# Kernel tuning notes

Hardware: AMD Instinct MI355X
Metric: run time of the kernel (lower is better)

Reference implementation:

```python
import jax, jax.numpy as jnp
import numpy as np

N_SRC = 50000
N_DST = 50000
E = 500000
H = 128
ED = 32
EPS = 1e-5


def _linear_params(key, fan_in, fan_out):
    kw, kb = jax.random.split(key)
    bound = 1.0 / np.sqrt(fan_in)
    W = jax.random.uniform(kw, (fan_in, fan_out), jnp.float32, -bound, bound)
    b = jax.random.uniform(kb, (fan_out,), jnp.float32, -bound, bound)
    return W, b


def setup_inputs() -> dict:
    key = jax.random.key(0)
    ks = jax.random.split(key, 12)
    src_x = jax.random.normal(ks[0], (N_SRC, H), jnp.float32)
    dst_x = jax.random.normal(ks[1], (N_DST, H), jnp.float32)
    edge_index = jax.random.randint(ks[2], (2, E), 0, N_DST, jnp.int64)
    edge_attr = jax.random.normal(ks[3], (E, ED), jnp.float32)
    Wsrc, bsrc = _linear_params(ks[4], H, H)
    Wdst, bdst = _linear_params(ks[5], H, H)
    We, be = _linear_params(ks[6], ED, H)
    Wattn, battn = _linear_params(ks[7], 3 * H, 1)
    Wmsg, bmsg = _linear_params(ks[8], H, H)
    Wout, bout = _linear_params(ks[9], 2 * H, H)
    gamma = jnp.ones((H,), jnp.float32)
    beta = jnp.zeros((H,), jnp.float32)
    return dict(src_x=src_x, dst_x=dst_x, edge_index=edge_index, edge_attr=edge_attr,
                Wsrc=Wsrc, bsrc=bsrc, Wdst=Wdst, bdst=bdst, We=We, be=be,
                Wattn=Wattn, battn=battn, Wmsg=Wmsg, bmsg=bmsg,
                Wout=Wout, bout=bout, gamma=gamma, beta=beta)


def _segment_softmax(scores, idx, num_segments):
    # numerically stable softmax over variable-size segments of dst index
    m = jax.ops.segment_max(scores, idx, num_segments=num_segments)
    ex = jnp.exp(scores - m[idx])
    s = jax.ops.segment_sum(ex, idx, num_segments=num_segments)
    return ex / s[idx]


def reference(src_x, dst_x, edge_index, edge_attr,
              Wsrc, bsrc, Wdst, bdst, We, be,
              Wattn, battn, Wmsg, bmsg, Wout, bout, gamma, beta):
    src_idx = edge_index[0]
    dst_idx = edge_index[1]
    num_dst = dst_x.shape[0]

    src_feat = src_x[src_idx] @ Wsrc + bsrc          # [E, H]
    dst_feat = dst_x[dst_idx] @ Wdst + bdst          # [E, H]
    e_feat = edge_attr @ We + be                     # [E, H]

    attn_in = jnp.concatenate([src_feat, dst_feat, e_feat], axis=-1)  # [E, 3H]
    msg = (src_feat + e_feat) @ Wmsg + bmsg          # [E, H]

    scores = (jnp.tanh(attn_in) @ Wattn + battn)[:, 0]  # [E]
    alpha = _segment_softmax(scores, dst_idx, num_dst)   # [E]

    agg = jax.ops.segment_sum(msg * alpha[:, None], dst_idx, num_segments=num_dst)  # [num_dst, H]

    updated = jnp.concatenate([dst_x, agg], axis=-1) @ Wout + bout
    # dropout is identity in eval mode
    h = dst_x + updated
    mu = jnp.mean(h, axis=-1, keepdims=True)
    var = jnp.var(h, axis=-1, keepdims=True)
    return (h - mu) * jax.lax.rsqrt(var + EPS) * gamma + beta
```

## Files before the change

kernel.cpp:

```cpp
#include <hip/hip_runtime.h>
#include <math.h>

#define NSRC 50000
#define NDST 50000
#define NE   500000
#define HD   128
#define EDIM 32
#define LN_EPS 1e-5f

typedef __attribute__((ext_vector_type(8))) short short8;
typedef __attribute__((ext_vector_type(4))) float f32x4;
typedef unsigned short u16;

#define TL2E 2.8853900817779268f
#define L2E  1.4426950408889634f

__device__ __forceinline__ float EXP2(float x) {
#if __has_builtin(__builtin_amdgcn_exp2f)
    return __builtin_amdgcn_exp2f(x);
#else
    return exp2f(x);
#endif
}
__device__ __forceinline__ float RCP(float x) {
#if __has_builtin(__builtin_amdgcn_rcpf)
    return __builtin_amdgcn_rcpf(x);
#else
    return 1.f / x;
#endif
}
__device__ __forceinline__ u16 f2b(float x) {
    unsigned u = __float_as_uint(x);
    return (u16)((u + 0x7FFFu + ((u >> 16) & 1u)) >> 16);
}
__device__ __forceinline__ float b2f(u16 h) {
    return __uint_as_float(((unsigned)h) << 16);
}
__device__ __forceinline__ short8 ld8(const u16* p) { return *(const short8*)p; }

__global__ __launch_bounds__(128) void fold1_kernel(
    const float* __restrict__ Wsrc, const float* __restrict__ bsrc,
    const float* __restrict__ We,   const float* __restrict__ be,
    const float* __restrict__ Wmsg, const float* __restrict__ bmsg,
    float* __restrict__ Wsm, float* __restrict__ bsm,
    float* __restrict__ WeMsg, float* __restrict__ c2)
{
    const int j = threadIdx.x;
    const int r = blockIdx.x;
    float s = 0.f;
    if (r < 128) {
        for (int k = 0; k < 128; ++k) s += Wsrc[r*HD + k] * Wmsg[k*HD + j];
        Wsm[r*HD + j] = s;
    } else if (r < 160) {
        const int rr = r - 128;
        for (int k = 0; k < 128; ++k) s += We[rr*HD + k] * Wmsg[k*HD + j];
        WeMsg[rr*HD + j] = s;
    } else if (r == 160) {
        for (int k = 0; k < 128; ++k) s += bsrc[k] * Wmsg[k*HD + j];
        bsm[j] = s + bmsg[j];
    } else {
        for (int k = 0; k < 128; ++k) s += be[k] * Wmsg[k*HD + j];
        c2[j] = s;
    }
}

__global__ __launch_bounds__(128) void fold2_kernel(
    const float* __restrict__ WeMsg, const float* __restrict__ c2,
    const float* __restrict__ Wout, const float* __restrict__ bout,
    float* __restrict__ W3, float* __restrict__ bias2,
    float* __restrict__ Wout1p)
{
    const int j = threadIdx.x;
    const int r = blockIdx.x;
    const float* Wout2 = Wout + HD*HD;
    if (r < 32) {
        float s = 0.f;
        for (int k = 0; k < 128; ++k) s += WeMsg[r*HD + k] * Wout2[k*HD + j];
        W3[r*HD + j] = s;
    } else if (r == 32) {
        float s = 0.f;
        for (int k = 0; k < 128; ++k) s += c2[k] * Wout2[k*HD + j];
        bias2[j] = s + bout[j];
    } else {
        const int rr = r - 33;
        Wout1p[rr*HD + j] = Wout[rr*HD + j] + ((rr == j) ? 1.f : 0.f);
    }
}

__global__ __launch_bounds__(64) void pack_all_kernel(
    const float* __restrict__ Wsrc, const float* __restrict__ Wdst,
    const float* __restrict__ Wsm,  const float* __restrict__ Wout1p,
    const float* __restrict__ Wout2,const float* __restrict__ We,
    const float* __restrict__ W3,
    u16* __restrict__ Wsrc_pk, u16* __restrict__ Wdst_pk,
    u16* __restrict__ Wsm_pk,  u16* __restrict__ W1_pk,
    u16* __restrict__ W2_pk,   u16* __restrict__ We_pk,
    u16* __restrict__ W3_pk)
{
    const int b = blockIdx.x;
    const int lane = threadIdx.x;
    const float* src; u16* dst; int lb; float scl = 1.f;
    if      (b < 32)  { src = Wsrc;   dst = Wsrc_pk; lb = b;       scl = TL2E; }
    else if (b < 64)  { src = Wdst;   dst = Wdst_pk; lb = b - 32;  scl = TL2E; }
    else if (b < 96)  { src = Wsm;    dst = Wsm_pk;  lb = b - 64; }
    else if (b < 128) { src = Wout1p; dst = W1_pk;   lb = b - 96; }
    else if (b < 160) { src = Wout2;  dst = W2_pk;   lb = b - 128; }
    else if (b < 168) { src = We;     dst = We_pk;   lb = b - 160; scl = TL2E; }
    else              { src = W3;     dst = W3_pk;   lb = b - 168; }
    const int kc = lb >> 3, t = lb & 7;
    const int ln = lane & 15, quad = lane >> 4;
    u16 tmp[8];
#pragma unroll
    for (int j = 0; j < 8; ++j)
        tmp[j] = f2b(src[(kc*32 + quad*8 + j)*HD + t*16 + ln] * scl);
    *(short8*)(dst + (size_t)(lb*64 + lane)*8) = *(short8*)tmp;
}

__global__ __launch_bounds__(256) void node_gemm_kernel(
    const float* __restrict__ src_x, const u16* __restrict__ Wsrc_pk,
    const u16* __restrict__ Wsm_pk, const float* __restrict__ bsrc,
    const float* __restrict__ bsm, const float* __restrict__ wa1,
    float* __restrict__ s1, u16* __restrict__ srcmsgb)
{
    __shared__ u16 lds[4 * 16 * HD];
    const int t = threadIdx.x;
    const int w = t >> 6, lane = t & 63;
    const int ln = lane & 15, quad = lane >> 4;
    int row0 = (blockIdx.x * 4 + w) * 16;
    if (row0 > NSRC - 16) row0 = NSRC - 16;

    const float* rp = src_x + (size_t)(row0 + ln)*HD;
    short8 a[4];
#pragma unroll
    for (int kc = 0; kc < 4; ++kc) {
        float4 f0 = *(const float4*)(rp + kc*32 + quad*8);
        float4 f1 = *(const float4*)(rp + kc*32 + quad*8 + 4);
        u16 tb[8] = { f2b(f0.x), f2b(f0.y), f2b(f0.z), f2b(f0.w),
                      f2b(f1.x), f2b(f1.y), f2b(f1.z), f2b(f1.w) };
        a[kc] = *(short8*)tb;
    }

    float v[4] = {0.f, 0.f, 0.f, 0.f};
    float ws = 0.f;
#pragma unroll
    for (int tt = 0; tt < 8; ++tt) {
        const float bb = bsrc[tt*16 + ln] * TL2E;
        const float ww = wa1[tt*16 + ln];
        f32x4 acc = {bb, bb, bb, bb};
#pragma unroll
        for (int kc = 0; kc < 4; ++kc) {
            short8 b = ld8(Wsrc_pk + (size_t)((kc*8 + tt)*64 + lane)*8);
            acc = __builtin_amdgcn_mfma_f32_16x16x32_bf16(a[kc], b, acc, 0, 0, 0);
        }
        ws += ww;
#pragma unroll
        for (int r = 0; r < 4; ++r)
            v[r] = fmaf(ww, RCP(EXP2(acc[r]) + 1.f), v[r]);
    }
#pragma unroll
    for (int off = 8; off >= 1; off >>= 1) {
        ws += __shfl_xor(ws, off);
#pragma unroll
        for (int r = 0; r < 4; ++r) v[r] += __shfl_xor(v[r], off);
    }
    if (ln == 0) {
#pragma unroll
        for (int r = 0; r < 4; ++r)
            s1[row0 + quad*4 + r] = fmaf(-2.f, v[r], ws);
    }

#pragma unroll
    for (int tt = 0; tt < 8; ++tt) {
        const float bs = bsm[tt*16 + ln];
        f32x4 acc = {bs, bs, bs, bs};
#pragma unroll
        for (int kc = 0; kc < 4; ++kc) {
            short8 b = ld8(Wsm_pk + (size_t)((kc*8 + tt)*64 + lane)*8);
            acc = __builtin_amdgcn_mfma_f32_16x16x32_bf16(a[kc], b, acc, 0, 0, 0);
        }
#pragma unroll
        for (int r = 0; r < 4; ++r)
            lds[w*2048 + (quad*4 + r)*HD + tt*16 + ln] = f2b(acc[r]);
    }
    __syncthreads();
#pragma unroll
    for (int r = 0; r < 4; ++r) {
        int idx = r*512 + lane*8;
        short8 val = *(short8*)(lds + w*2048 + idx);
        int row = idx >> 7, col = idx & 127;
        *(short8*)(srcmsgb + (size_t)(row0 + row)*HD + col) = val;
    }
}

__global__ __launch_bounds__(256) void dst_gemm_kernel(
    const float* __restrict__ dst_x, const u16* __restrict__ Wdst_pk,
    const float* __restrict__ bdst, const float* __restrict__ wa2,
    float* __restrict__ s2)
{
    const int t = threadIdx.x;
    const int w = t >> 6, lane = t & 63;
    const int ln = lane & 15, quad = lane >> 4;
    int row0 = (blockIdx.x * 4 + w) * 16;
    if (row0 > NDST - 16) row0 = NDST - 16;

    const float* rp = dst_x + (size_t)(row0 + ln)*HD;
    short8 a[4];
#pragma unroll
    for (int kc = 0; kc < 4; ++kc) {
        float4 f0 = *(const float4*)(rp + kc*32 + quad*8);
        float4 f1 = *(const float4*)(rp + kc*32 + quad*8 + 4);
        u16 tb[8] = { f2b(f0.x), f2b(f0.y), f2b(f0.z), f2b(f0.w),
                      f2b(f1.x), f2b(f1.y), f2b(f1.z), f2b(f1.w) };
        a[kc] = *(short8*)tb;
    }

    float v[4] = {0.f, 0.f, 0.f, 0.f};
    float ws = 0.f;
#pragma unroll
    for (int tt = 0; tt < 8; ++tt) {
        const float bb = bdst[tt*16 + ln] * TL2E;
        const float ww = wa2[tt*16 + ln];
        f32x4 acc = {bb, bb, bb, bb};
#pragma unroll
        for (int kc = 0; kc < 4; ++kc) {
            short8 b = ld8(Wdst_pk + (size_t)((kc*8 + tt)*64 + lane)*8);
            acc = __builtin_amdgcn_mfma_f32_16x16x32_bf16(a[kc], b, acc, 0, 0, 0);
        }
        ws += ww;
#pragma unroll
        for (int r = 0; r < 4; ++r)
            v[r] = fmaf(ww, RCP(EXP2(acc[r]) + 1.f), v[r]);
    }
#pragma unroll
    for (int off = 8; off >= 1; off >>= 1) {
        ws += __shfl_xor(ws, off);
#pragma unroll
        for (int r = 0; r < 4; ++r) v[r] += __shfl_xor(v[r], off);
    }
    if (ln == 0) {
#pragma unroll
        for (int r = 0; r < 4; ++r)
            s2[row0 + quad*4 + r] = fmaf(-2.f, v[r], ws);
    }
}

__global__ void hist_kernel(const int* __restrict__ ei, int* __restrict__ cnt)
{
    int e = blockIdx.x * 256 + threadIdx.x;
    if (e < NE) atomicAdd(&cnt[ei[NE + e]], 1);
}

__global__ __launch_bounds__(1024) void scan1_kernel(
    const int* __restrict__ cnt, int* __restrict__ excl, int* __restrict__ bsum)
{
    __shared__ int buf[1024];
    const int t = threadIdx.x;
    const int i = blockIdx.x * 1024 + t;
    int v = (i < NDST) ? cnt[i] : 0;
    buf[t] = v;
    __syncthreads();
    for (int off = 1; off < 1024; off <<= 1) {
        int tv = (t >= off) ? buf[t - off] : 0;
        __syncthreads();
        buf[t] += tv;
        __syncthreads();
    }
    if (i < NDST) excl[i] = buf[t] - v;
    if (t == 1023) bsum[blockIdx.x] = buf[1023];
}

__global__ void scan2_kernel(int* __restrict__ bsum, int* __restrict__ rowptr)
{
    const int NB = (NDST + 1023) / 1024;
    const int t = threadIdx.x;
    int orig = (t < NB) ? bsum[t] : 0;
    int v = orig;
    for (int off = 1; off < 64; off <<= 1) {
        int u = __shfl_up(v, off);
        if (t >= off) v += u;
    }
    int total = __shfl(v, 63);
    if (t < NB) bsum[t] = v - orig;
    if (t == 0) rowptr[NDST] = total;
}

__global__ void scan3_kernel(const int* __restrict__ bsum,
                             int* __restrict__ rowptr, int* __restrict__ cursor)
{
    int i = blockIdx.x * 256 + threadIdx.x;
    if (i < NDST) {
        int v = rowptr[i] + bsum[i >> 10];
        rowptr[i] = v;
        cursor[i] = v;
    }
}

__global__ __launch_bounds__(256) void edge_score_kernel(
    const int* __restrict__ ei, const float* __restrict__ eattr,
    const u16* __restrict__ We_pk, const float* __restrict__ be,
    const float* __restrict__ wattn, const float* __restrict__ battn,
    const float* __restrict__ s1, const float* __restrict__ s2,
    int* __restrict__ cursor, int2* __restrict__ ev8, u16* __restrict__ eas)
{
    const int t = threadIdx.x;
    const int w = t >> 6, lane = t & 63;
    const int ln = lane & 15, quad = lane >> 4;
    const int e0 = (blockIdx.x * 4 + w) * 16;
    if (e0 >= NE) return;

    const float* ap = eattr + (size_t)(e0 + ln)*EDIM + quad*8;
    float4 f0 = *(const float4*)(ap);
    float4 f1 = *(const float4*)(ap + 4);
    u16 ab[8] = { f2b(f0.x), f2b(f0.y), f2b(f0.z), f2b(f0.w),
                  f2b(f1.x), f2b(f1.y), f2b(f1.z), f2b(f1.w) };
    short8 a = *(short8*)ab;

    const float* wa3 = wattn + 2*HD;
    float v[4] = {0.f, 0.f, 0.f, 0.f};
    float ws = 0.f;
#pragma unroll
    for (int tt = 0; tt < 8; ++tt) {
        const float bb = be[tt*16 + ln] * TL2E;
        const float ww = wa3[tt*16 + ln];
        f32x4 acc = {bb, bb, bb, bb};
        short8 b = ld8(We_pk + (size_t)(tt*64 + lane)*8);
        acc = __builtin_amdgcn_mfma_f32_16x16x32_bf16(a, b, acc, 0, 0, 0);
        ws += ww;
#pragma unroll
        for (int r = 0; r < 4; ++r)
            v[r] = fmaf(ww, RCP(EXP2(acc[r]) + 1.f), v[r]);
    }
#pragma unroll
    for (int off = 8; off >= 1; off >>= 1) {
        ws += __shfl_xor(ws, off);
#pragma unroll
        for (int r = 0; r < 4; ++r) v[r] += __shfl_xor(v[r], off);
    }
    const int srcq = (ln >> 2) << 4;
    float sv0 = __shfl(v[0], srcq);
    float sv1 = __shfl(v[1], srcq);
    float sv2 = __shfl(v[2], srcq);
    float sv3 = __shfl(v[3], srcq);
    const int rr = ln & 3;
    float vlo = (rr & 1) ? sv1 : sv0;
    float vhi = (rr & 1) ? sv3 : sv2;
    float vv  = (rr & 2) ? vhi : vlo;

    int pos;
    if (quad == 0) {
        const int e = e0 + ln;
        const int srcn = ei[e];
        const int dstn = ei[NE + e];
        float sc = (fmaf(-2.f, vv, ws) + s1[srcn] + s2[dstn] + battn[0]) * L2E;
        pos = atomicAdd(&cursor[dstn], 1);
        ev8[pos] = make_int2(srcn, __float_as_int(sc));
    }
    pos = __shfl(pos, ln);
    *(short8*)(eas + (size_t)pos*EDIM + quad*8) = a;
}

__global__ __launch_bounds__(256) void dst_agg_kernel(
    const int2* __restrict__ ev8, const u16* __restrict__ eas,
    const int* __restrict__ rowptr, const u16* __restrict__ srcmsgb,
    const float* __restrict__ c2,
    u16* __restrict__ aggSb, u16* __restrict__ weab)
{
    const int lane = threadIdx.x & 63;
    const int d = blockIdx.x * 4 + (threadIdx.x >> 6);
    const int el = lane >> 4, c = lane & 15;
    const int start = rowptr[d], end = rowptr[d + 1];

    if (start == end) {
        if (el == 0) {
            u16 z[8];
#pragma unroll
            for (int j = 0; j < 8; ++j) z[j] = f2b(-c2[c*8 + j]);
            *(short8*)(aggSb + (size_t)d*HD + c*8) = *(short8*)z;
            if (c < 4) {
                u16 zz[8] = {0,0,0,0,0,0,0,0};
                *(short8*)(weab + (size_t)d*EDIM + c*8) = *(short8*)zz;
            }
        }
        return;
    }

    float sacc = 0.f;
    float acc[8]  = {0,0,0,0,0,0,0,0};
    float wacc[8] = {0,0,0,0,0,0,0,0};

    int icur = start + el;
    bool vcur = (icur < end);
    int iicur = vcur ? icur : start;
    int2 q = ev8[iicur];

    for (int i0 = start; i0 < end; i0 += 4) {
        const float wgt = vcur ? EXP2(__int_as_float(q.y)) : 0.f;
        const int   srow = q.x;
        const int   iiuse = iicur;
        const int inx = i0 + 4 + el;
        vcur = (inx < end);
        iicur = vcur ? inx : start;
        q = ev8[iicur];

        sacc += wgt;
        short8 sm = ld8(srcmsgb + (size_t)srow*HD + c*8);
#pragma unroll
        for (int j = 0; j < 8; ++j)
            acc[j] = fmaf(wgt, b2f(((u16*)&sm)[j]), acc[j]);
        if (c < 4) {
            short8 eav = ld8(eas + (size_t)iiuse*EDIM + c*8);
#pragma unroll
            for (int j = 0; j < 8; ++j)
                wacc[j] = fmaf(wgt, b2f(((u16*)&eav)[j]), wacc[j]);
        }
    }
#pragma unroll
    for (int off = 16; off <= 32; off <<= 1) {
        sacc += __shfl_xor(sacc, off);
#pragma unroll
        for (int j = 0; j < 8; ++j) {
            acc[j]  += __shfl_xor(acc[j],  off);
            wacc[j] += __shfl_xor(wacc[j], off);
        }
    }
    const float inv = RCP(sacc);
    if (el == 0) {
        u16 o[8];
#pragma unroll
        for (int j = 0; j < 8; ++j) o[j] = f2b(acc[j] * inv);
        *(short8*)(aggSb + (size_t)d*HD + c*8) = *(short8*)o;
        if (c < 4) {
            u16 o2[8];
#pragma unroll
            for (int j = 0; j < 8; ++j) o2[j] = f2b(wacc[j] * inv);
            *(short8*)(weab + (size_t)d*EDIM + c*8) = *(short8*)o2;
        }
    }
}

__global__ __launch_bounds__(256) void final_kernel(
    const float* __restrict__ dst_x, const u16* __restrict__ aggSb,
    const u16* __restrict__ weab,
    const u16* __restrict__ W1_pk, const u16* __restrict__ W2_pk,
    const u16* __restrict__ W3_pk, const float* __restrict__ bias2,
    const float* __restrict__ gamma, const float* __restrict__ beta,
    float* __restrict__ out)
{
    const int t = threadIdx.x;
    const int w = t >> 6, lane = t & 63;
    const int ln = lane & 15, quad = lane >> 4;
    int row0 = (blockIdx.x * 4 + w) * 16;
    if (row0 > NDST - 16) row0 = NDST - 16;

    const float* rp = dst_x + (size_t)(row0 + ln)*HD;
    short8 a1[4], a2[4], a3;
#pragma unroll
    for (int kc = 0; kc < 4; ++kc) {
        float4 f0 = *(const float4*)(rp + kc*32 + quad*8);
        float4 f1 = *(const float4*)(rp + kc*32 + quad*8 + 4);
        u16 tb[8] = { f2b(f0.x), f2b(f0.y), f2b(f0.z), f2b(f0.w),
                      f2b(f1.x), f2b(f1.y), f2b(f1.z), f2b(f1.w) };
        a1[kc] = *(short8*)tb;
        a2[kc] = ld8(aggSb + (size_t)(row0 + ln)*HD + kc*32 + quad*8);
    }
    a3 = ld8(weab + (size_t)(row0 + ln)*EDIM + quad*8);

    f32x4 accs[8];
#pragma unroll
    for (int tt = 0; tt < 8; ++tt) {
        const float bb = bias2[tt*16 + ln];
        f32x4 acc = {bb, bb, bb, bb};
#pragma unroll
        for (int kc = 0; kc < 4; ++kc) {
            short8 b = ld8(W1_pk + (size_t)((kc*8 + tt)*64 + lane)*8);
            acc = __builtin_amdgcn_mfma_f32_16x16x32_bf16(a1[kc], b, acc, 0, 0, 0);
        }
#pragma unroll
        for (int kc = 0; kc < 4; ++kc) {
            short8 b = ld8(W2_pk + (size_t)((kc*8 + tt)*64 + lane)*8);
            acc = __builtin_amdgcn_mfma_f32_16x16x32_bf16(a2[kc], b, acc, 0, 0, 0);
        }
        {
            short8 b = ld8(W3_pk + (size_t)(tt*64 + lane)*8);
            acc = __builtin_amdgcn_mfma_f32_16x16x32_bf16(a3, b, acc, 0, 0, 0);
        }
        accs[tt] = acc;
    }

    const float gl[8] = { gamma[ln], gamma[16+ln], gamma[32+ln], gamma[48+ln],
                          gamma[64+ln], gamma[80+ln], gamma[96+ln], gamma[112+ln] };
    const float bl[8] = { beta[ln], beta[16+ln], beta[32+ln], beta[48+ln],
                          beta[64+ln], beta[80+ln], beta[96+ln], beta[112+ln] };
#pragma unroll
    for (int r = 0; r < 4; ++r) {
        float s = 0.f, qq = 0.f;
#pragma unroll
        for (int tt = 0; tt < 8; ++tt) {
            float u = accs[tt][r];
            s += u; qq += u*u;
        }
#pragma unroll
        for (int off = 8; off >= 1; off >>= 1) {
            s  += __shfl_xor(s, off);
            qq += __shfl_xor(qq, off);
        }
        const float mean = s * (1.f / HD);
        const float var  = qq * (1.f / HD) - mean * mean;
        const float rstd = rsqrtf(var + LN_EPS);
        const int row = row0 + quad*4 + r;
#pragma unroll
        for (int tt = 0; tt < 8; ++tt)
            out[(size_t)row*HD + tt*16 + ln] =
                (accs[tt][r] - mean) * rstd * gl[tt] + bl[tt];
    }
}

extern "C" void kernel_launch(void* const* d_in, const int* in_sizes, int n_in,
                              void* d_out, int out_size, void* d_ws, size_t ws_size,
                              hipStream_t stream)
{
    const float* src_x = (const float*)d_in[0];
    const float* dst_x = (const float*)d_in[1];
    const int*   ei    = (const int*)d_in[2];
    const float* eattr = (const float*)d_in[3];
    const float* Wsrc  = (const float*)d_in[4];
    const float* bsrc  = (const float*)d_in[5];
    const float* Wdst  = (const float*)d_in[6];
    const float* bdst  = (const float*)d_in[7];
    const float* We    = (const float*)d_in[8];
    const float* be    = (const float*)d_in[9];
    const float* Wattn = (const float*)d_in[10];
    const float* battn = (const float*)d_in[11];
    const float* Wmsg  = (const float*)d_in[12];
    const float* bmsg  = (const float*)d_in[13];
    const float* Wout  = (const float*)d_in[14];
    const float* bout  = (const float*)d_in[15];
    const float* gamma = (const float*)d_in[16];
    const float* beta  = (const float*)d_in[17];
    float* out = (float*)d_out;

    float* ws = (float*)d_ws;
    u16* srcmsgb = (u16*)(ws + 0);
    u16* aggSb   = (u16*)(ws + 3200000);
    u16* weab    = (u16*)(ws + 6400000);
    u16* eas     = (u16*)(ws + 7200000);
    float* s1    = ws + 15200000;
    float* s2    = ws + 15250048;
    float* Wsm   = ws + 15300096;
    float* bsm   = ws + 15316480;
    float* WeMsg = ws + 15316608;
    float* c2    = ws + 15320704;
    float* W3    = ws + 15320832;
    float* bias2 = ws + 15324928;
    float* Wout1p= ws + 15325056;
    u16* Wsrc_pk = (u16*)(ws + 15341440);
    u16* Wdst_pk = (u16*)(ws + 15349632);
    u16* Wsm_pk  = (u16*)(ws + 15357824);
    u16* W1_pk   = (u16*)(ws + 15366016);
    u16* W2_pk   = (u16*)(ws + 15374208);
    u16* We_pk   = (u16*)(ws + 15382400);
    u16* W3_pk   = (u16*)(ws + 15384448);
    int* rowptr  = (int*)(ws + 15386496);
    int* cursor  = rowptr + 50016;
    int* bsum    = cursor + 50016;
    int2* ev8    = (int2*)(bsum + 64);

    hipMemsetAsync(cursor, 0, NDST * sizeof(int), stream);

    fold1_kernel<<<162, 128, 0, stream>>>(Wsrc, bsrc, We, be, Wmsg, bmsg,
                                          Wsm, bsm, WeMsg, c2);
    fold2_kernel<<<161, 128, 0, stream>>>(WeMsg, c2, Wout, bout, W3, bias2, Wout1p);
    pack_all_kernel<<<176, 64, 0, stream>>>(Wsrc, Wdst, Wsm, Wout1p, Wout + HD*HD,
                                            We, W3,
                                            Wsrc_pk, Wdst_pk, Wsm_pk, W1_pk,
                                            W2_pk, We_pk, W3_pk);

    const int g16 = (NSRC/16 + 3) / 4;

    node_gemm_kernel<<<g16, 256, 0, stream>>>(src_x, Wsrc_pk, Wsm_pk, bsrc, bsm,
                                              Wattn, s1, srcmsgb);
    dst_gemm_kernel<<<g16, 256, 0, stream>>>(dst_x, Wdst_pk, bdst, Wattn + HD, s2);

    hist_kernel<<<(NE + 255) / 256, 256, 0, stream>>>(ei, cursor);
    scan1_kernel<<<(NDST + 1023) / 1024, 1024, 0, stream>>>(cursor, rowptr, bsum);
    scan2_kernel<<<1, 64, 0, stream>>>(bsum, rowptr);
    scan3_kernel<<<(NDST + 255) / 256, 256, 0, stream>>>(bsum, rowptr, cursor);

    edge_score_kernel<<<(NE/16 + 3) / 4, 256, 0, stream>>>(
        ei, eattr, We_pk, be, Wattn, battn, s1, s2, cursor, ev8, eas);

    dst_agg_kernel<<<NDST / 4, 256, 0, stream>>>(ev8, eas, rowptr, srcmsgb,
                                                 c2, aggSb, weab);

    final_kernel<<<g16, 256, 0, stream>>>(dst_x, aggSb, weab, W1_pk, W2_pk, W3_pk,
                                          bias2, gamma, beta, out);
}
```

Before: 337.6 us.

## Merge node GEMMs and histogram into one kernel, drop edge-attr scatter buffer

Folds fold2 into the pack kernel and moves the count-buffer zeroing into fold1, replacing the memset. It merges the src and dst node GEMMs and the degree histogram into one launch, with the histogram recording a per-edge rank. Scan2 and scan3 are merged into one kernel. Edge scoring now writes (src, edge id, score) to a deterministic position given by rowptr plus rank, with no atomic cursor. The aggregation kernel reads fp32 edge_attr directly by edge id instead of a scattered bf16 copy. The aim is fewer launches and less scatter traffic, at the cost of a random gather of edge_attr rows during aggregation.

```diff
diff --git a/kernel.cpp b/kernel.cpp
--- a/kernel.cpp
+++ b/kernel.cpp
@@ -43,10 +43,16 @@
     const float* __restrict__ We,   const float* __restrict__ be,
     const float* __restrict__ Wmsg, const float* __restrict__ bmsg,
     float* __restrict__ Wsm, float* __restrict__ bsm,
-    float* __restrict__ WeMsg, float* __restrict__ c2)
+    float* __restrict__ WeMsg, float* __restrict__ c2,
+    int* __restrict__ cnt)
 {
     const int j = threadIdx.x;
     const int r = blockIdx.x;
+    if (r >= 162) {
+        int i = (r - 162) * 128 + j;
+        if (i < NDST + 16) cnt[i] = 0;
+        return;
+    }
     float s = 0.f;
     if (r < 128) {
         for (int k = 0; k < 128; ++k) s += Wsrc[r*HD + k] * Wmsg[k*HD + j];
@@ -64,93 +70,124 @@
     }
 }
 
-__global__ __launch_bounds__(128) void fold2_kernel(
-    const float* __restrict__ WeMsg, const float* __restrict__ c2,
-    const float* __restrict__ Wout, const float* __restrict__ bout,
-    float* __restrict__ W3, float* __restrict__ bias2,
-    float* __restrict__ Wout1p)
-{
-    const int j = threadIdx.x;
-    const int r = blockIdx.x;
-    const float* Wout2 = Wout + HD*HD;
-    if (r < 32) {
-        float s = 0.f;
-        for (int k = 0; k < 128; ++k) s += WeMsg[r*HD + k] * Wout2[k*HD + j];
-        W3[r*HD + j] = s;
-    } else if (r == 32) {
-        float s = 0.f;
-        for (int k = 0; k < 128; ++k) s += c2[k] * Wout2[k*HD + j];
-        bias2[j] = s + bout[j];
-    } else {
-        const int rr = r - 33;
-        Wout1p[rr*HD + j] = Wout[rr*HD + j] + ((rr == j) ? 1.f : 0.f);
-    }
-}
-
 __global__ __launch_bounds__(64) void pack_all_kernel(
     const float* __restrict__ Wsrc, const float* __restrict__ Wdst,
-    const float* __restrict__ Wsm,  const float* __restrict__ Wout1p,
-    const float* __restrict__ Wout2,const float* __restrict__ We,
-    const float* __restrict__ W3,
+    const float* __restrict__ Wsm,  const float* __restrict__ Wout,
+    const float* __restrict__ We,   const float* __restrict__ WeMsg,
+    const float* __restrict__ c2,   const float* __restrict__ bout,
     u16* __restrict__ Wsrc_pk, u16* __restrict__ Wdst_pk,
     u16* __restrict__ Wsm_pk,  u16* __restrict__ W1_pk,
     u16* __restrict__ W2_pk,   u16* __restrict__ We_pk,
-    u16* __restrict__ W3_pk)
+    u16* __restrict__ W3_pk,   float* __restrict__ bias2)
 {
     const int b = blockIdx.x;
     const int lane = threadIdx.x;
-    const float* src; u16* dst; int lb; float scl = 1.f;
-    if      (b < 32)  { src = Wsrc;   dst = Wsrc_pk; lb = b;       scl = TL2E; }
-    else if (b < 64)  { src = Wdst;   dst = Wdst_pk; lb = b - 32;  scl = TL2E; }
-    else if (b < 96)  { src = Wsm;    dst = Wsm_pk;  lb = b - 64; }
-    else if (b < 128) { src = Wout1p; dst = W1_pk;   lb = b - 96; }
-    else if (b < 160) { src = Wout2;  dst = W2_pk;   lb = b - 128; }
-    else if (b < 168) { src = We;     dst = We_pk;   lb = b - 160; scl = TL2E; }
-    else              { src = W3;     dst = W3_pk;   lb = b - 168; }
+    const int ln = lane & 15, quad = lane >> 4;
+    const float* Wout2 = Wout + HD*HD;
+
+    if (b == 176) {
+#pragma unroll
+        for (int h = 0; h < 2; ++h) {
+            const int col = lane + h*64;
+            float s = 0.f;
+            for (int k = 0; k < 128; ++k) s += c2[k] * Wout2[k*HD + col];
+            bias2[col] = bout[col] + s;
+        }
+        return;
+    }
+    if (b >= 168) {
+        const int t = b - 168;
+        const int jj = t*16 + ln;
+        float sacc[8] = {0,0,0,0,0,0,0,0};
+        for (int k = 0; k < 128; ++k) {
+            const float w2 = Wout2[k*HD + jj];
+#pragma unroll
+            for (int j = 0; j < 8; ++j)
+                sacc[j] = fmaf(WeMsg[(quad*8 + j)*HD + k], w2, sacc[j]);
+        }
+        u16 tmp[8];
+#pragma unroll
+        for (int j = 0; j < 8; ++j) tmp[j] = f2b(sacc[j]);
+        *(short8*)(W3_pk + (size_t)(t*64 + lane)*8) = *(short8*)tmp;
+        return;
+    }
+
+    const float* src; u16* dst; int lb; float scl = 1.f; bool addI = false;
+    if      (b < 32)  { src = Wsrc; dst = Wsrc_pk; lb = b;       scl = TL2E; }
+    else if (b < 64)  { src = Wdst; dst = Wdst_pk; lb = b - 32;  scl = TL2E; }
+    else if (b < 96)  { src = Wsm;  dst = Wsm_pk;  lb = b - 64; }
+    else if (b < 128) { src = Wout; dst = W1_pk;   lb = b - 96;  addI = true; }
+    else if (b < 160) { src = Wout2;dst = W2_pk;   lb = b - 128; }
+    else              { src = We;   dst = We_pk;   lb = b - 160; scl = TL2E; }
     const int kc = lb >> 3, t = lb & 7;
-    const int ln = lane & 15, quad = lane >> 4;
     u16 tmp[8];
 #pragma unroll
-    for (int j = 0; j < 8; ++j)
-        tmp[j] = f2b(src[(kc*32 + quad*8 + j)*HD + t*16 + ln] * scl);
+    for (int j = 0; j < 8; ++j) {
+        const int i = kc*32 + quad*8 + j, jj = t*16 + ln;
+        float v = src[(size_t)i*HD + jj] * scl;
+        if (addI && i == jj) v += 1.f;
+        tmp[j] = f2b(v);
+    }
     *(short8*)(dst + (size_t)(lb*64 + lane)*8) = *(short8*)tmp;
 }
 
-__global__ __launch_bounds__(256) void node_gemm_kernel(
-    const float* __restrict__ src_x, const u16* __restrict__ Wsrc_pk,
-    const u16* __restrict__ Wsm_pk, const float* __restrict__ bsrc,
-    const float* __restrict__ bsm, const float* __restrict__ wa1,
-    float* __restrict__ s1, u16* __restrict__ srcmsgb)
+#define GN 782
+#define HB ((NE + 255) / 256)
+
+__global__ __launch_bounds__(256) void mega_kernel(
+    const float* __restrict__ src_x, const float* __restrict__ dst_x,
+    const int* __restrict__ ei,
+    const u16* __restrict__ Wsrc_pk, const u16* __restrict__ Wsm_pk,
+    const u16* __restrict__ Wdst_pk,
+    const float* __restrict__ bsrc, const float* __restrict__ bsm,
+    const float* __restrict__ bdst, const float* __restrict__ wattn,
+    float* __restrict__ s1, float* __restrict__ s2,
+    u16* __restrict__ srcmsgb, int* __restrict__ cnt, int* __restrict__ rank)
 {
     __shared__ u16 lds[4 * 16 * HD];
     const int t = threadIdx.x;
+    const int blk = blockIdx.x;
+
+    if (blk >= 2*GN) {
+        const int e = (blk - 2*GN) * 256 + t;
+        if (e < NE) rank[e] = atomicAdd(&cnt[ei[NE + e]], 1);
+        return;
+    }
+
     const int w = t >> 6, lane = t & 63;
     const int ln = lane & 15, quad = lane >> 4;
-    int row0 = (blockIdx.x * 4 + w) * 16;
+    const bool is_src = (blk < GN);
+    const int b = is_src ? blk : blk - GN;
+    int row0 = (b * 4 + w) * 16;
     if (row0 > NSRC - 16) row0 = NSRC - 16;
 
-    const float* rp = src_x + (size_t)(row0 + ln)*HD;
+    const float* xp = (is_src ? src_x : dst_x) + (size_t)(row0 + ln)*HD;
     short8 a[4];
 #pragma unroll
     for (int kc = 0; kc < 4; ++kc) {
-        float4 f0 = *(const float4*)(rp + kc*32 + quad*8);
-        float4 f1 = *(const float4*)(rp + kc*32 + quad*8 + 4);
+        float4 f0 = *(const float4*)(xp + kc*32 + quad*8);
+        float4 f1 = *(const float4*)(xp + kc*32 + quad*8 + 4);
         u16 tb[8] = { f2b(f0.x), f2b(f0.y), f2b(f0.z), f2b(f0.w),
                       f2b(f1.x), f2b(f1.y), f2b(f1.z), f2b(f1.w) };
         a[kc] = *(short8*)tb;
     }
 
+    const u16*   Wpk = is_src ? Wsrc_pk : Wdst_pk;
+    const float* bb_ = is_src ? bsrc : bdst;
+    const float* wa  = is_src ? wattn : wattn + HD;
+    float* sout      = is_src ? s1 : s2;
+
     float v[4] = {0.f, 0.f, 0.f, 0.f};
     float ws = 0.f;
 #pragma unroll
     for (int tt = 0; tt < 8; ++tt) {
-        const float bb = bsrc[tt*16 + ln] * TL2E;
-        const float ww = wa1[tt*16 + ln];
+        const float bb = bb_[tt*16 + ln] * TL2E;
+        const float ww = wa[tt*16 + ln];
         f32x4 acc = {bb, bb, bb, bb};
 #pragma unroll
         for (int kc = 0; kc < 4; ++kc) {
-            short8 b = ld8(Wsrc_pk + (size_t)((kc*8 + tt)*64 + lane)*8);
-            acc = __builtin_amdgcn_mfma_f32_16x16x32_bf16(a[kc], b, acc, 0, 0, 0);
+            short8 bfr = ld8(Wpk + (size_t)((kc*8 + tt)*64 + lane)*8);
+            acc = __builtin_amdgcn_mfma_f32_16x16x32_bf16(a[kc], bfr, acc, 0, 0, 0);
         }
         ws += ww;
 #pragma unroll
@@ -166,8 +203,10 @@
     if (ln == 0) {
 #pragma unroll
         for (int r = 0; r < 4; ++r)
-            s1[row0 + quad*4 + r] = fmaf(-2.f, v[r], ws);
-    }
+            sout[row0 + quad*4 + r] = fmaf(-2.f, v[r], ws);
+    }
+
+    if (!is_src) return;
 
 #pragma unroll
     for (int tt = 0; tt < 8; ++tt) {
@@ -175,8 +214,8 @@
         f32x4 acc = {bs, bs, bs, bs};
 #pragma unroll
         for (int kc = 0; kc < 4; ++kc) {
-            short8 b = ld8(Wsm_pk + (size_t)((kc*8 + tt)*64 + lane)*8);
-            acc = __builtin_amdgcn_mfma_f32_16x16x32_bf16(a[kc], b, acc, 0, 0, 0);
+            short8 bfr = ld8(Wsm_pk + (size_t)((kc*8 + tt)*64 + lane)*8);
+            acc = __builtin_amdgcn_mfma_f32_16x16x32_bf16(a[kc], bfr, acc, 0, 0, 0);
         }
 #pragma unroll
         for (int r = 0; r < 4; ++r)
@@ -190,64 +229,6 @@
         int row = idx >> 7, col = idx & 127;
         *(short8*)(srcmsgb + (size_t)(row0 + row)*HD + col) = val;
     }
-}
-
-__global__ __launch_bounds__(256) void dst_gemm_kernel(
-    const float* __restrict__ dst_x, const u16* __restrict__ Wdst_pk,
-    const float* __restrict__ bdst, const float* __restrict__ wa2,
-    float* __restrict__ s2)
-{
-    const int t = threadIdx.x;
-    const int w = t >> 6, lane = t & 63;
-    const int ln = lane & 15, quad = lane >> 4;
-    int row0 = (blockIdx.x * 4 + w) * 16;
-    if (row0 > NDST - 16) row0 = NDST - 16;
-
-    const float* rp = dst_x + (size_t)(row0 + ln)*HD;
-    short8 a[4];
-#pragma unroll
-    for (int kc = 0; kc < 4; ++kc) {
-        float4 f0 = *(const float4*)(rp + kc*32 + quad*8);
-        float4 f1 = *(const float4*)(rp + kc*32 + quad*8 + 4);
-        u16 tb[8] = { f2b(f0.x), f2b(f0.y), f2b(f0.z), f2b(f0.w),
-                      f2b(f1.x), f2b(f1.y), f2b(f1.z), f2b(f1.w) };
-        a[kc] = *(short8*)tb;
-    }
-
-    float v[4] = {0.f, 0.f, 0.f, 0.f};
-    float ws = 0.f;
-#pragma unroll
-    for (int tt = 0; tt < 8; ++tt) {
-        const float bb = bdst[tt*16 + ln] * TL2E;
-        const float ww = wa2[tt*16 + ln];
-        f32x4 acc = {bb, bb, bb, bb};
-#pragma unroll
-        for (int kc = 0; kc < 4; ++kc) {
-            short8 b = ld8(Wdst_pk + (size_t)((kc*8 + tt)*64 + lane)*8);
-            acc = __builtin_amdgcn_mfma_f32_16x16x32_bf16(a[kc], b, acc, 0, 0, 0);
-        }
-        ws += ww;
-#pragma unroll
-        for (int r = 0; r < 4; ++r)
-            v[r] = fmaf(ww, RCP(EXP2(acc[r]) + 1.f), v[r]);
-    }
-#pragma unroll
-    for (int off = 8; off >= 1; off >>= 1) {
-        ws += __shfl_xor(ws, off);
-#pragma unroll
-        for (int r = 0; r < 4; ++r) v[r] += __shfl_xor(v[r], off);
-    }
-    if (ln == 0) {
-#pragma unroll
-        for (int r = 0; r < 4; ++r)
-            s2[row0 + quad*4 + r] = fmaf(-2.f, v[r], ws);
-    }
-}
-
-__global__ void hist_kernel(const int* __restrict__ ei, int* __restrict__ cnt)
-{
-    int e = blockIdx.x * 256 + threadIdx.x;
-    if (e < NE) atomicAdd(&cnt[ei[NE + e]], 1);
 }
 
 __global__ __launch_bounds__(1024) void scan1_kernel(
@@ -269,30 +250,25 @@
     if (t == 1023) bsum[blockIdx.x] = buf[1023];
 }
 
-__global__ void scan2_kernel(int* __restrict__ bsum, int* __restrict__ rowptr)
-{
+__global__ __launch_bounds__(256) void scan23_kernel(
+    const int* __restrict__ bsum, int* __restrict__ rowptr)
+{
+    __shared__ int pref[64];
+    const int t = threadIdx.x;
     const int NB = (NDST + 1023) / 1024;
-    const int t = threadIdx.x;
-    int orig = (t < NB) ? bsum[t] : 0;
-    int v = orig;
-    for (int off = 1; off < 64; off <<= 1) {
-        int u = __shfl_up(v, off);
-        if (t >= off) v += u;
-    }
-    int total = __shfl(v, 63);
-    if (t < NB) bsum[t] = v - orig;
-    if (t == 0) rowptr[NDST] = total;
-}
-
-__global__ void scan3_kernel(const int* __restrict__ bsum,
-                             int* __restrict__ rowptr, int* __restrict__ cursor)
-{
-    int i = blockIdx.x * 256 + threadIdx.x;
-    if (i < NDST) {
-        int v = rowptr[i] + bsum[i >> 10];
-        rowptr[i] = v;
-        cursor[i] = v;
-    }
+    if (t < 64) {
+        int orig = (t < NB) ? bsum[t] : 0;
+        int v = orig;
+        for (int off = 1; off < 64; off <<= 1) {
+            int u = __shfl_up(v, off);
+            if (t >= off) v += u;
+        }
+        pref[t] = v - orig;
+        if (blockIdx.x == 0 && t == NB - 1) rowptr[NDST] = v;
+    }
+    __syncthreads();
+    const int i = blockIdx.x * 256 + t;
+    if (i < NDST) rowptr[i] += pref[i >> 10];
 }
 
 __global__ __launch_bounds__(256) void edge_score_kernel(
@@ -300,7 +276,8 @@
     const u16* __restrict__ We_pk, const float* __restrict__ be,
     const float* __restrict__ wattn, const float* __restrict__ battn,
     const float* __restrict__ s1, const float* __restrict__ s2,
-    int* __restrict__ cursor, int2* __restrict__ ev8, u16* __restrict__ eas)
+    const int* __restrict__ rowptr, const int* __restrict__ rank,
+    int4* __restrict__ ev16)
 {
     const int t = threadIdx.x;
     const int w = t >> 6, lane = t & 63;
@@ -346,22 +323,19 @@
     float vhi = (rr & 1) ? sv3 : sv2;
     float vv  = (rr & 2) ? vhi : vlo;
 
-    int pos;
     if (quad == 0) {
         const int e = e0 + ln;
         const int srcn = ei[e];
         const int dstn = ei[NE + e];
         float sc = (fmaf(-2.f, vv, ws) + s1[srcn] + s2[dstn] + battn[0]) * L2E;
-        pos = atomicAdd(&cursor[dstn], 1);
-        ev8[pos] = make_int2(srcn, __float_as_int(sc));
-    }
-    pos = __shfl(pos, ln);
-    *(short8*)(eas + (size_t)pos*EDIM + quad*8) = a;
+        const int pos = rowptr[dstn] + rank[e];
+        ev16[pos] = make_int4(srcn, e, __float_as_int(sc), 0);
+    }
 }
 
 __global__ __launch_bounds__(256) void dst_agg_kernel(
-    const int2* __restrict__ ev8, const u16* __restrict__ eas,
-    const int* __restrict__ rowptr, const u16* __restrict__ srcmsgb,
+    const int4* __restrict__ ev16, const int* __restrict__ rowptr,
+    const u16* __restrict__ srcmsgb, const float* __restrict__ eattr,
     const float* __restrict__ c2,
     u16* __restrict__ aggSb, u16* __restrict__ weab)
 {
@@ -376,9 +350,9 @@
 #pragma unroll
             for (int j = 0; j < 8; ++j) z[j] = f2b(-c2[c*8 + j]);
             *(short8*)(aggSb + (size_t)d*HD + c*8) = *(short8*)z;
-            if (c < 4) {
-                u16 zz[8] = {0,0,0,0,0,0,0,0};
-                *(short8*)(weab + (size_t)d*EDIM + c*8) = *(short8*)zz;
+            if (c < 8) {
+                u16 zz[4] = {0,0,0,0};
+                *(ushort4*)(weab + (size_t)d*EDIM + c*4) = *(ushort4*)zz;
             }
         }
         return;
@@ -386,42 +360,42 @@
 
     float sacc = 0.f;
     float acc[8]  = {0,0,0,0,0,0,0,0};
-    float wacc[8] = {0,0,0,0,0,0,0,0};
+    float wacc[4] = {0,0,0,0};
 
     int icur = start + el;
     bool vcur = (icur < end);
     int iicur = vcur ? icur : start;
-    int2 q = ev8[iicur];
+    int4 q = ev16[iicur];
 
     for (int i0 = start; i0 < end; i0 += 4) {
-        const float wgt = vcur ? EXP2(__int_as_float(q.y)) : 0.f;
+        const float wgt = vcur ? EXP2(__int_as_float(q.z)) : 0.f;
         const int   srow = q.x;
-        const int   iiuse = iicur;
+        const int   ecur = q.y;
         const int inx = i0 + 4 + el;
         vcur = (inx < end);
         iicur = vcur ? inx : start;
-        q = ev8[iicur];
+        q = ev16[iicur];
 
         sacc += wgt;
         short8 sm = ld8(srcmsgb + (size_t)srow*HD + c*8);
 #pragma unroll
         for (int j = 0; j < 8; ++j)
             acc[j] = fmaf(wgt, b2f(((u16*)&sm)[j]), acc[j]);
-        if (c < 4) {
-            short8 eav = ld8(eas + (size_t)iiuse*EDIM + c*8);
-#pragma unroll
-            for (int j = 0; j < 8; ++j)
-                wacc[j] = fmaf(wgt, b2f(((u16*)&eav)[j]), wacc[j]);
+        if (c < 8) {
+            float4 f = *(const float4*)(eattr + (size_t)ecur*EDIM + c*4);
+            wacc[0] = fmaf(wgt, f.x, wacc[0]);
+            wacc[1] = fmaf(wgt, f.y, wacc[1]);
+            wacc[2] = fmaf(wgt, f.z, wacc[2]);
+            wacc[3] = fmaf(wgt, f.w, wacc[3]);
         }
     }
 #pragma unroll
     for (int off = 16; off <= 32; off <<= 1) {
         sacc += __shfl_xor(sacc, off);
 #pragma unroll
-        for (int j = 0; j < 8; ++j) {
-            acc[j]  += __shfl_xor(acc[j],  off);
-            wacc[j] += __shfl_xor(wacc[j], off);
-        }
+        for (int j = 0; j < 8; ++j) acc[j] += __shfl_xor(acc[j], off);
+#pragma unroll
+        for (int j = 0; j < 4; ++j) wacc[j] += __shfl_xor(wacc[j], off);
     }
     const float inv = RCP(sacc);
     if (el == 0) {
@@ -429,11 +403,11 @@
 #pragma unroll
         for (int j = 0; j < 8; ++j) o[j] = f2b(acc[j] * inv);
         *(short8*)(aggSb + (size_t)d*HD + c*8) = *(short8*)o;
-        if (c < 4) {
-            u16 o2[8];
-#pragma unroll
-            for (int j = 0; j < 8; ++j) o2[j] = f2b(wacc[j] * inv);
-            *(short8*)(weab + (size_t)d*EDIM + c*8) = *(short8*)o2;
+        if (c < 8) {
+            u16 o2[4];
+#pragma unroll
+            for (int j = 0; j < 4; ++j) o2[j] = f2b(wacc[j] * inv);
+            *(ushort4*)(weab + (size_t)d*EDIM + c*4) = *(ushort4*)o2;
         }
     }
 }
@@ -543,55 +517,46 @@
     u16* srcmsgb = (u16*)(ws + 0);
     u16* aggSb   = (u16*)(ws + 3200000);
     u16* weab    = (u16*)(ws + 6400000);
-    u16* eas     = (u16*)(ws + 7200000);
-    float* s1    = ws + 15200000;
-    float* s2    = ws + 15250048;
-    float* Wsm   = ws + 15300096;
-    float* bsm   = ws + 15316480;
-    float* WeMsg = ws + 15316608;
-    float* c2    = ws + 15320704;
-    float* W3    = ws + 15320832;
-    float* bias2 = ws + 15324928;
-    float* Wout1p= ws + 15325056;
-    u16* Wsrc_pk = (u16*)(ws + 15341440);
-    u16* Wdst_pk = (u16*)(ws + 15349632);
-    u16* Wsm_pk  = (u16*)(ws + 15357824);
-    u16* W1_pk   = (u16*)(ws + 15366016);
-    u16* W2_pk   = (u16*)(ws + 15374208);
-    u16* We_pk   = (u16*)(ws + 15382400);
-    u16* W3_pk   = (u16*)(ws + 15384448);
-    int* rowptr  = (int*)(ws + 15386496);
-    int* cursor  = rowptr + 50016;
-    int* bsum    = cursor + 50016;
-    int2* ev8    = (int2*)(bsum + 64);
-
-    hipMemsetAsync(cursor, 0, NDST * sizeof(int), stream);
-
-    fold1_kernel<<<162, 128, 0, stream>>>(Wsrc, bsrc, We, be, Wmsg, bmsg,
-                                          Wsm, bsm, WeMsg, c2);
-    fold2_kernel<<<161, 128, 0, stream>>>(WeMsg, c2, Wout, bout, W3, bias2, Wout1p);
-    pack_all_kernel<<<176, 64, 0, stream>>>(Wsrc, Wdst, Wsm, Wout1p, Wout + HD*HD,
-                                            We, W3,
+    float* s1    = ws + 7200000;
+    float* s2    = ws + 7250048;
+    float* Wsm   = ws + 7300096;
+    float* bsm   = ws + 7316480;
+    float* WeMsg = ws + 7316608;
+    float* c2    = ws + 7320704;
+    float* bias2 = ws + 7320832;
+    u16* Wsrc_pk = (u16*)(ws + 7320960);
+    u16* Wdst_pk = (u16*)(ws + 7329152);
+    u16* Wsm_pk  = (u16*)(ws + 7337344);
+    u16* W1_pk   = (u16*)(ws + 7345536);
+    u16* W2_pk   = (u16*)(ws + 7353728);
+    u16* We_pk   = (u16*)(ws + 7361920);
+    u16* W3_pk   = (u16*)(ws + 7363968);
+    int* rowptr  = (int*)(ws + 7366016);
+    int* cnt     = (int*)(ws + 7416032);
+    int* bsum    = (int*)(ws + 7466048);
+    int* rank    = (int*)(ws + 7466112);
+    int4* ev16   = (int4*)(ws + 7966112);
+
+    fold1_kernel<<<553, 128, 0, stream>>>(Wsrc, bsrc, We, be, Wmsg, bmsg,
+                                          Wsm, bsm, WeMsg, c2, cnt);
+    pack_all_kernel<<<177, 64, 0, stream>>>(Wsrc, Wdst, Wsm, Wout, We, WeMsg,
+                                            c2, bout,
                                             Wsrc_pk, Wdst_pk, Wsm_pk, W1_pk,
-                                            W2_pk, We_pk, W3_pk);
-
-    const int g16 = (NSRC/16 + 3) / 4;
-
-    node_gemm_kernel<<<g16, 256, 0, stream>>>(src_x, Wsrc_pk, Wsm_pk, bsrc, bsm,
-                                              Wattn, s1, srcmsgb);
-    dst_gemm_kernel<<<g16, 256, 0, stream>>>(dst_x, Wdst_pk, bdst, Wattn + HD, s2);
-
-    hist_kernel<<<(NE + 255) / 256, 256, 0, stream>>>(ei, cursor);
-    scan1_kernel<<<(NDST + 1023) / 1024, 1024, 0, stream>>>(cursor, rowptr, bsum);
-    scan2_kernel<<<1, 64, 0, stream>>>(bsum, rowptr);
-    scan3_kernel<<<(NDST + 255) / 256, 256, 0, stream>>>(bsum, rowptr, cursor);
+                                            W2_pk, We_pk, W3_pk, bias2);
+
+    mega_kernel<<<2*GN + HB, 256, 0, stream>>>(
+        src_x, dst_x, ei, Wsrc_pk, Wsm_pk, Wdst_pk,
+        bsrc, bsm, bdst, Wattn, s1, s2, srcmsgb, cnt, rank);
+
+    scan1_kernel<<<(NDST + 1023) / 1024, 1024, 0, stream>>>(cnt, rowptr, bsum);
+    scan23_kernel<<<(NDST + 255) / 256, 256, 0, stream>>>(bsum, rowptr);
 
     edge_score_kernel<<<(NE/16 + 3) / 4, 256, 0, stream>>>(
-        ei, eattr, We_pk, be, Wattn, battn, s1, s2, cursor, ev8, eas);
-
-    dst_agg_kernel<<<NDST / 4, 256, 0, stream>>>(ev8, eas, rowptr, srcmsgb,
-                                                 c2, aggSb, weab);
-
-    final_kernel<<<g16, 256, 0, stream>>>(dst_x, aggSb, weab, W1_pk, W2_pk, W3_pk,
-                                          bias2, gamma, beta, out);
-}
+        ei, eattr, We_pk, be, Wattn, battn, s1, s2, rowptr, rank, ev16);
+
+    dst_agg_kernel<<<NDST / 4, 256, 0, stream>>>(ev16, rowptr, srcmsgb,
+                                                 eattr, c2, aggSb, weab);
+
+    final_kernel<<<GN, 256, 0, stream>>>(dst_x, aggSb, weab, W1_pk, W2_pk, W3_pk,
+                                         bias2, gamma, beta, out);
+}
```

Result: faster. 305.8 us (-9.4%).
